# Performance work log

Hardware: AMD Instinct MI355X
Metric: run time of the kernel (lower is better)

## Reference

```python
import jax, jax.numpy as jnp
import numpy as np

N, B, T, C = 1024, 4, 12, 64
D, H, K, E = 64, 2, 3, 16384  # out_dim, gat heads, num_kernel, edges per kernel
NEG_SLOPE_ATTN = 0.2   # DGL GATConv default
NEG_SLOPE_ACT = 0.01   # nn.LeakyReLU default


def setup_inputs() -> dict:
    key = jax.random.key(0)
    ks = jax.random.split(key, 12)
    input_feature = jax.random.normal(ks[0], (B, N, T, C), dtype=jnp.float32)
    # edge lists per kernel, with self loops appended (dgl.add_self_loop)
    loops = jnp.broadcast_to(jnp.arange(N, dtype=jnp.int32), (K, N))
    src_idx = jnp.concatenate(
        [jax.random.randint(ks[1], (K, E), 0, N, dtype=jnp.int32), loops], axis=1)
    dst_idx = jnp.concatenate(
        [jax.random.randint(ks[2], (K, E), 0, N, dtype=jnp.int32), loops], axis=1)
    # GATConv params per kernel: fc (no bias), attn_l/attn_r, output bias
    fc_w = jax.random.normal(ks[3], (K, C, H * D), dtype=jnp.float32) * 0.1
    attn_l = jax.random.normal(ks[4], (K, H, D), dtype=jnp.float32) * 0.1
    attn_r = jax.random.normal(ks[5], (K, H, D), dtype=jnp.float32) * 0.1
    gat_bias = jax.random.normal(ks[6], (K, H * D), dtype=jnp.float32) * 0.02
    # per-kernel merge weight, init std 0.05 as in init_weight()
    weight = jax.random.normal(ks[7], (K,), dtype=jnp.float32) * 0.05
    # merge MLP: Linear(H*D -> D)
    merge_w = jax.random.normal(ks[8], (H * D, D), dtype=jnp.float32) * 0.05
    merge_b = jax.random.normal(ks[9], (D,), dtype=jnp.float32) * 0.02
    return {"input_feature": input_feature, "fc_w": fc_w, "attn_l": attn_l,
            "attn_r": attn_r, "gat_bias": gat_bias, "weight": weight,
            "merge_w": merge_w, "merge_b": merge_b,
            "src_idx": src_idx, "dst_idx": dst_idx}


def _gat_conv(x, fc_w, attn_l, attn_r, bias, src, dst):
    """DGL GATConv on feature x: [N,B,T,C] -> [N,B,T,H,D]."""
    feat = jnp.einsum('nbtc,ce->nbte', x, fc_w).reshape(N, B, T, H, D)
    el = jnp.einsum('nbthd,hd->nbth', feat, attn_l)  # [N,B,T,H]
    er = jnp.einsum('nbthd,hd->nbth', feat, attn_r)
    e = jax.nn.leaky_relu(el[src] + er[dst], NEG_SLOPE_ATTN)  # [Etot,B,T,H]
    # segment softmax over destination neighborhoods (self loops guarantee >=1 edge)
    emax = jax.ops.segment_max(e, dst, num_segments=N)
    a = jnp.exp(e - emax[dst])
    denom = jax.ops.segment_sum(a, dst, num_segments=N)
    alpha = a / denom[dst]
    msg = alpha[..., None] * feat[src]  # [Etot,B,T,H,D]
    rst = jax.ops.segment_sum(msg, dst, num_segments=N)
    return rst + bias.reshape(H, D)


def reference(input_feature, fc_w, attn_l, attn_r, gat_bias, weight,
              merge_w, merge_b, src_idx, dst_idx):
    x = jnp.transpose(input_feature, (1, 0, 2, 3))  # [N,B,T,C]
    result = jnp.zeros((N, B, T, H, D), dtype=x.dtype)
    for i in range(K):  # small fixed set of dilated kernels
        result = result + weight[i] * _gat_conv(
            x, fc_w[i], attn_l[i], attn_r[i], gat_bias[i], src_idx[i], dst_idx[i])
    merged = result.reshape(N, B, T, H * D) @ merge_w + merge_b  # [N,B,T,D]
    out = jax.nn.leaky_relu(merged, NEG_SLOPE_ACT) + x  # residual = Identity (C==D)
    return jnp.transpose(out, (1, 0, 2, 3))  # [B,N,T,D]
```

## Files before the change

kernel.cpp:

```cpp
#include <hip/hip_runtime.h>

#define NN   1024
#define TT   12
#define CC   64
#define DD   64
#define HH   2
#define KK   3
#define ETOT 17408
#define BT   48
#define BTH  96
#define HD   128
#define NODES (KK * NN + 1)
#define PADN  (KK * NN)
#define CSR_CAP (KK * ETOT + 12 * NN)
#define LOG2E 1.44269504f
#define MT   128
#define NBLK (NN * BT / MT)
#define EDGE_BLOCKS ((KK * ETOT + 255) / 256)
#define FEAT_BLOCKS (KK * NBLK)
#define NSL  12
#define RUNCAP 144

typedef __attribute__((ext_vector_type(8))) short s8v;
typedef __attribute__((ext_vector_type(4))) float f4v;

__device__ __forceinline__ float bf_lo(unsigned int u) {
    return __uint_as_float(u << 16);
}
__device__ __forceinline__ float bf_hi(unsigned int u) {
    return __uint_as_float(u & 0xFFFF0000u);
}
__device__ __forceinline__ unsigned short f2bf(float f) {
    unsigned int u = __float_as_uint(f);
    u += 0x7FFFu + ((u >> 16) & 1u);
    return (unsigned short)(u >> 16);
}
__device__ __forceinline__ unsigned int pack2(float a, float b) {
    return (unsigned int)f2bf(a) | ((unsigned int)f2bf(b) << 16);
}
__device__ __forceinline__ float rlf(float v, int lane) {
    return __int_as_float(__builtin_amdgcn_readlane(__float_as_int(v), lane));
}

__global__ __launch_bounds__(256) void aux_kernel(
    const int* __restrict__ dst_idx, int* __restrict__ counts,
    const float* __restrict__ fc_w, const float* __restrict__ attn_l,
    const float* __restrict__ attn_r, float* __restrict__ alc, float* __restrict__ arc,
    uint4* __restrict__ featp, float* __restrict__ elp)
{
    int bid = blockIdx.x;
    int t = threadIdx.x;
    if (bid < EDGE_BLOCKS) {
        int tid = bid * 256 + t;
        if (tid < KK * ETOT) {
            int k = tid / ETOT;
            atomicAdd(&counts[k * NN + dst_idx[tid]], 1);
        }
    } else {
        for (int item = t; item < KK * HH * CC; item += 256) {
            int kh = item >> 6, c = item & 63;
            int k = kh >> 1, h = kh & 1;
            float sl = 0.f, sr = 0.f;
            #pragma unroll
            for (int dd = 0; dd < 64; ++dd) {
                float wv = fc_w[k * CC * HD + c * HD + h * 64 + dd];
                sl = fmaf(wv, attn_l[k * HD + h * 64 + dd], sl);
                sr = fmaf(wv, attn_r[k * HD + h * 64 + dd], sr);
            }
            alc[item] = sl * LOG2E;
            arc[item] = sr * LOG2E;
        }
        for (int item = t; item < NSL * 64; item += 256)
            featp[((size_t)(item >> 6) * NODES + PADN) * 64 + (item & 63)] =
                make_uint4(0u, 0u, 0u, 0u);
        for (int item = t; item < NSL * 8; item += 256)
            elp[((size_t)(item >> 3) * NODES + PADN) * 8 + (item & 7)] = -1e30f;
    }
}

__global__ __launch_bounds__(1024) void scan_kernel(
    const int* __restrict__ counts,
    int4* __restrict__ segs, int* __restrict__ cursor, int* __restrict__ csr_comb)
{
    int n = threadIdx.x;
    int c0 = counts[n], c1 = counts[NN + n], c2 = counts[2 * NN + n];
    int p0 = (c0 + 3) & ~3, p1 = (c1 + 3) & ~3, p2 = (c2 + 3) & ~3;
    int tot = p0 + p1 + p2;
    __shared__ int buf[NN];
    buf[n] = tot;
    __syncthreads();
    for (int off = 1; off < NN; off <<= 1) {
        int v = (n >= off) ? buf[n - off] : 0;
        __syncthreads();
        buf[n] += v;
        __syncthreads();
    }
    int excl = buf[n] - tot;
    int4 sg;
    sg.x = excl; sg.y = excl + p0; sg.z = excl + p0 + p1; sg.w = excl + tot;
    segs[n] = sg;
    cursor[n] = sg.x;
    cursor[NN + n] = sg.y;
    cursor[2 * NN + n] = sg.z;
    for (int j = sg.x + c0; j < sg.y; ++j) csr_comb[j] = PADN;
    for (int j = sg.y + c1; j < sg.z; ++j) csr_comb[j] = PADN;
    for (int j = sg.z + c2; j < sg.w; ++j) csr_comb[j] = PADN;
}

__global__ __launch_bounds__(256) void feat_kernel(
    const float* __restrict__ x, const float* __restrict__ fc_w,
    uint4* __restrict__ featp)
{
    int kb = blockIdx.x;
    int k  = kb / NBLK;
    int m0 = (kb - k * NBLK) * MT;
    int t  = threadIdx.x;
    int w  = t >> 6, l = t & 63;

    __shared__ __align__(16) unsigned short As[128 * 64];
    __shared__ __align__(16) unsigned short Ws[128 * 64];

    #pragma unroll
    for (int rep = 0; rep < 4; ++rep) {
        int gid = t + 256 * rep;
        int row = gid >> 3, g = gid & 7;
        int m = m0 + row;
        int n = m / BT, bt = m - n * BT;
        int b = bt / TT, tt2 = bt - b * TT;
        const float* xr = &x[(((size_t)b * NN + n) * TT + tt2) * CC + g * 8];
        float4 v0 = *(const float4*)xr;
        float4 v1 = *(const float4*)(xr + 4);
        uint4 pk = { pack2(v0.x, v0.y), pack2(v0.z, v0.w),
                     pack2(v1.x, v1.y), pack2(v1.z, v1.w) };
        *(uint4*)((char*)As + row * 128 + ((g ^ (row & 7)) << 4)) = pk;
    }
    #pragma unroll
    for (int rep = 0; rep < 4; ++rep) {
        int gid = t + 256 * rep;
        int e = gid & 127, g = gid >> 7;
        float v[8];
        #pragma unroll
        for (int jj = 0; jj < 8; ++jj)
            v[jj] = fc_w[(size_t)k * CC * HD + (g * 8 + jj) * HD + e];
        uint4 pk = { pack2(v[0], v[1]), pack2(v[2], v[3]),
                     pack2(v[4], v[5]), pack2(v[6], v[7]) };
        *(uint4*)((char*)Ws + e * 128 + ((g ^ (e & 7)) << 4)) = pk;
    }
    __syncthreads();

    int Mw = (w & 1) * 64;
    int Nw = (w >> 1) * 64;
    int rsel = l & 15, ksel = l >> 4;

    f4v acc[4][4];
    #pragma unroll
    for (int mi = 0; mi < 4; ++mi)
        #pragma unroll
        for (int nf = 0; nf < 4; ++nf)
            acc[mi][nf] = (f4v){0.f, 0.f, 0.f, 0.f};

    s8v af[4][2], bf[4][2];
    #pragma unroll
    for (int mi = 0; mi < 4; ++mi)
        #pragma unroll
        for (int ks = 0; ks < 2; ++ks) {
            int row = Mw + mi * 16 + rsel;
            int g = ks * 4 + ksel;
            af[mi][ks] = *(const s8v*)((const char*)As + row * 128 + ((g ^ (row & 7)) << 4));
        }
    #pragma unroll
    for (int nf = 0; nf < 4; ++nf)
        #pragma unroll
        for (int ks = 0; ks < 2; ++ks) {
            int e = Nw + nf * 16 + rsel;
            int g = ks * 4 + ksel;
            bf[nf][ks] = *(const s8v*)((const char*)Ws + e * 128 + ((g ^ (e & 7)) << 4));
        }

    #pragma unroll
    for (int mi = 0; mi < 4; ++mi)
        #pragma unroll
        for (int nf = 0; nf < 4; ++nf) {
            acc[mi][nf] = __builtin_amdgcn_mfma_f32_16x16x32_bf16(
                af[mi][0], bf[nf][0], acc[mi][nf], 0, 0, 0);
            acc[mi][nf] = __builtin_amdgcn_mfma_f32_16x16x32_bf16(
                af[mi][1], bf[nf][1], acc[mi][nf], 0, 0, 0);
        }

    int i0 = (l >> 4) * 4;
    bool writer = ((l >> 4) & 1) == 0;
    #pragma unroll
    for (int mi = 0; mi < 4; ++mi) {
        int m = m0 + Mw + mi * 16 + i0;
        int n = m / BT, bt = m - n * BT;
        #pragma unroll
        for (int nf = 0; nf < 4; ++nf) {
            uint2 o = { pack2(acc[mi][nf][0], acc[mi][nf][1]),
                        pack2(acc[mi][nf][2], acc[mi][nf][3]) };
            unsigned int px = (unsigned int)__shfl_xor((int)o.x, 16, 64);
            unsigned int py = (unsigned int)__shfl_xor((int)o.y, 16, 64);
            if (writer) {
                int e = Nw + nf * 16 + (l & 15);
                int h = e >> 6, d = e & 63;
                int s = ((bt >> 3) << 1) + h;
                featp[((size_t)s * NODES + k * NN + n) * 64 + d] =
                    make_uint4(o.x, o.y, px, py);
            }
        }
    }
}

__global__ __launch_bounds__(256) void side_kernel(
    const int* __restrict__ src_idx, const int* __restrict__ dst_idx,
    int* __restrict__ cursor, int* __restrict__ csr_comb,
    const float* __restrict__ x,
    const float* __restrict__ alc, const float* __restrict__ arc,
    float* __restrict__ elp, float* __restrict__ er)
{
    int bid = blockIdx.x;
    int t = threadIdx.x;

    if (bid < EDGE_BLOCKS) {
        int tid = bid * 256 + t;
        if (tid < KK * ETOT) {
            int k = tid / ETOT;
            int pos = atomicAdd(&cursor[k * NN + dst_idx[tid]], 1);
            csr_comb[pos] = k * NN + src_idx[tid];
        }
        return;
    }

    __shared__ float x_lds[BT * CC];
    __shared__ float cl[KK * HH * CC];
    __shared__ float cr[KK * HH * CC];
    int n = bid - EDGE_BLOCKS;

    for (int i = t; i < BT * CC; i += 256) {
        int bt = i >> 6, c = i & 63;
        int b = bt / TT, tt = bt - b * TT;
        x_lds[i] = x[(((size_t)b * NN + n) * TT + tt) * CC + c];
    }
    for (int i = t; i < KK * HH * CC; i += 256) { cl[i] = alc[i]; cr[i] = arc[i]; }
    __syncthreads();

    if (t < BTH) {
        int hh = t / BT, bt = t - hh * BT;
        #pragma unroll
        for (int k = 0; k < KK; ++k) {
            const float* alp = &cl[(k * HH + hh) * CC];
            const float* arp = &cr[(k * HH + hh) * CC];
            float sl = 0.f, sr = 0.f;
            #pragma unroll
            for (int cc = 0; cc < CC; ++cc) {
                int c = (cc + bt) & 63;
                float xv = x_lds[bt * CC + c];
                sl = fmaf(xv, alp[c], sl);
                sr = fmaf(xv, arp[c], sr);
            }
            int s = ((bt >> 3) << 1) + hh;
            elp[((size_t)s * NODES + k * NN + n) * 8 + (bt & 7)] = sl;
            er[((size_t)(k * NN + n)) * BTH + t] = sr;
        }
    }
}

#define EFMA(F, LO, HI)                                        \
    r0 = fmaf((LO).x, bf_lo((F).x), r0);                       \
    r1 = fmaf((LO).y, bf_hi((F).x), r1);                       \
    r2 = fmaf((LO).z, bf_lo((F).y), r2);                       \
    r3 = fmaf((LO).w, bf_hi((F).y), r3);                       \
    r4 = fmaf((HI).x, bf_lo((F).z), r4);                       \
    r5 = fmaf((HI).y, bf_hi((F).z), r5);                       \
    r6 = fmaf((HI).z, bf_lo((F).w), r6);                       \
    r7 = fmaf((HI).w, bf_hi((F).w), r7);

#define PHASE1(JB, JE, KIDX, SCLO, SCHI) {                                     \
    int jb = (JB), je = (JE);                                                  \
    float erv = er[((size_t)((KIDX) * NN + n)) * BTH + h * BT + btg8 * 8 + btq];\
    float ss = 0.f;                                                            \
    for (int j0 = jb; j0 < je; j0 += 8) {                                      \
        int jj = j0 + joff;                                                    \
        float a = 0.f;                                                         \
        if (jj < je) {                                                         \
            int idx = csr_comb[jj];                                            \
            float ev = elp[(size_t)sbase8 + (size_t)idx * 8 + btq] + erv;      \
            ev = fmaxf(ev, ev * 0.2f);                                         \
            a = __builtin_amdgcn_exp2f(ev);                                    \
            alds[w][jj - base0][btq] = a;                                      \
        }                                                                      \
        ss += a;                                                               \
    }                                                                          \
    ss += __shfl_xor(ss, 8, 64);                                               \
    ss += __shfl_xor(ss, 16, 64);                                              \
    ss += __shfl_xor(ss, 32, 64);                                              \
    float wk_ = weight[KIDX];                                                  \
    SCLO = make_float4(wk_ * __builtin_amdgcn_rcpf(rlf(ss, 0)),                \
                       wk_ * __builtin_amdgcn_rcpf(rlf(ss, 1)),                \
                       wk_ * __builtin_amdgcn_rcpf(rlf(ss, 2)),                \
                       wk_ * __builtin_amdgcn_rcpf(rlf(ss, 3)));               \
    SCHI = make_float4(wk_ * __builtin_amdgcn_rcpf(rlf(ss, 4)),                \
                       wk_ * __builtin_amdgcn_rcpf(rlf(ss, 5)),                \
                       wk_ * __builtin_amdgcn_rcpf(rlf(ss, 6)),                \
                       wk_ * __builtin_amdgcn_rcpf(rlf(ss, 7))); }

#define PHASE2(JB, JE, SCLO, SCHI) {                                           \
    int jb = __builtin_amdgcn_readfirstlane(JB);                               \
    int je = __builtin_amdgcn_readfirstlane(JE);                               \
    float r0=0.f,r1=0.f,r2=0.f,r3=0.f,r4=0.f,r5=0.f,r6=0.f,r7=0.f;             \
    for (int jj = jb; jj < je; jj += 4) {                                      \
        int4 i4 = *(const int4*)&csr_comb[jj];                                 \
        int i0 = __builtin_amdgcn_readfirstlane(i4.x);                         \
        int i1 = __builtin_amdgcn_readfirstlane(i4.y);                         \
        int i2 = __builtin_amdgcn_readfirstlane(i4.z);                         \
        int i3 = __builtin_amdgcn_readfirstlane(i4.w);                         \
        uint4 f0 = fb[(size_t)i0 * 64];                                        \
        uint4 f1 = fb[(size_t)i1 * 64];                                        \
        uint4 f2 = fb[(size_t)i2 * 64];                                        \
        uint4 f3 = fb[(size_t)i3 * 64];                                        \
        float4 L0 = *(const float4*)&alds[w][jj - base0 + 0][0];               \
        float4 H0 = *(const float4*)&alds[w][jj - base0 + 0][4];               \
        float4 L1 = *(const float4*)&alds[w][jj - base0 + 1][0];               \
        float4 H1 = *(const float4*)&alds[w][jj - base0 + 1][4];               \
        float4 L2 = *(const float4*)&alds[w][jj - base0 + 2][0];               \
        float4 H2 = *(const float4*)&alds[w][jj - base0 + 2][4];               \
        float4 L3 = *(const float4*)&alds[w][jj - base0 + 3][0];               \
        float4 H3 = *(const float4*)&alds[w][jj - base0 + 3][4];               \
        EFMA(f0, L0, H0); EFMA(f1, L1, H1);                                    \
        EFMA(f2, L2, H2); EFMA(f3, L3, H3);                                    \
    }                                                                          \
    acc0 = fmaf(r0, (SCLO).x, acc0); acc1 = fmaf(r1, (SCLO).y, acc1);          \
    acc2 = fmaf(r2, (SCLO).z, acc2); acc3 = fmaf(r3, (SCLO).w, acc3);          \
    acc4 = fmaf(r4, (SCHI).x, acc4); acc5 = fmaf(r5, (SCHI).y, acc5);          \
    acc6 = fmaf(r6, (SCHI).z, acc6); acc7 = fmaf(r7, (SCHI).w, acc7); }

__global__ __launch_bounds__(256) void agg_kernel(
    const uint4* __restrict__ featp,
    const float* __restrict__ elp,
    const float* __restrict__ er,
    const int4* __restrict__ segs, const int* __restrict__ csr_comb,
    const float* __restrict__ gat_bias, const float* __restrict__ weight,
    unsigned short* __restrict__ gatb)
{
    int xcd = (int)blockIdx.x & 7;
    int q   = (int)blockIdx.x >> 3;
    int j   = q + 384 * xcd;
    int s   = j >> 8;
    int g   = j & 255;
    int w = threadIdx.x >> 6;
    int l = threadIdx.x & 63;
    int n = g * 4 + w;
    int btg8 = s >> 1, h = s & 1;
    int e = h * 64 + l;

    __shared__ __align__(16) float alds[4][RUNCAP][8];

    const uint4* fb = featp + (size_t)s * NODES * 64 + l;
    size_t sbase8 = (size_t)s * NODES * 8;
    int4 sg = segs[n];
    int base0 = __builtin_amdgcn_readfirstlane(sg.x);

    int joff = l >> 3, btq = l & 7;
    float acc0=0.f,acc1=0.f,acc2=0.f,acc3=0.f,acc4=0.f,acc5=0.f,acc6=0.f,acc7=0.f;
    float4 sclo, schi;

    PHASE1(sg.x, sg.y, 0, sclo, schi)
    PHASE2(sg.x, sg.y, sclo, schi)
    PHASE1(sg.y, sg.z, 1, sclo, schi)
    PHASE2(sg.y, sg.z, sclo, schi)
    PHASE1(sg.z, sg.w, 2, sclo, schi)
    PHASE2(sg.z, sg.w, sclo, schi)

    float wb = weight[0] * gat_bias[e] + weight[1] * gat_bias[HD + e]
             + weight[2] * gat_bias[2 * HD + e];
    acc0 += wb; acc1 += wb; acc2 += wb; acc3 += wb;
    acc4 += wb; acc5 += wb; acc6 += wb; acc7 += wb;

    size_t row = (size_t)n * BT + btg8 * 8;
    gatb[(row + 0) * HD + e] = f2bf(acc0);
    gatb[(row + 1) * HD + e] = f2bf(acc1);
    gatb[(row + 2) * HD + e] = f2bf(acc2);
    gatb[(row + 3) * HD + e] = f2bf(acc3);
    gatb[(row + 4) * HD + e] = f2bf(acc4);
    gatb[(row + 5) * HD + e] = f2bf(acc5);
    gatb[(row + 6) * HD + e] = f2bf(acc6);
    gatb[(row + 7) * HD + e] = f2bf(acc7);
}
#undef EFMA
#undef PHASE1
#undef PHASE2

__global__ __launch_bounds__(256) void merge_mfma_kernel(
    const unsigned short* __restrict__ gatb,
    const float* __restrict__ merge_w, const float* __restrict__ merge_b,
    const float* __restrict__ x, float* __restrict__ out)
{
    int m0 = blockIdx.x * 128;
    int t = threadIdx.x, w = t >> 6, l = t & 63;

    __shared__ __align__(16) unsigned short As[128 * 128];
    __shared__ __align__(16) unsigned short Bs[64 * 128];

    #pragma unroll
    for (int rep = 0; rep < 8; ++rep) {
        int gid = t + 256 * rep;
        int row = gid >> 4, gg = gid & 15;
        uint4 v = *(const uint4*)((const char*)gatb + ((size_t)(m0 + row)) * 256 + gg * 16);
        *(uint4*)((char*)As + row * 256 + ((gg ^ (row & 15)) << 4)) = v;
    }
    #pragma unroll
    for (int rep = 0; rep < 4; ++rep) {
        int gid = t + 256 * rep;
        int col = gid >> 4, gg = gid & 15;
        float v[8];
        #pragma unroll
        for (int jj = 0; jj < 8; ++jj)
            v[jj] = merge_w[(gg * 8 + jj) * DD + col];
        uint4 pk = { pack2(v[0], v[1]), pack2(v[2], v[3]),
                     pack2(v[4], v[5]), pack2(v[6], v[7]) };
        *(uint4*)((char*)Bs + col * 256 + ((gg ^ (col & 15)) << 4)) = pk;
    }
    __syncthreads();

    int Mw = (w & 1) * 64, Nw = (w >> 1) * 32;
    int rsel = l & 15, ksel = l >> 4;

    f4v acc[4][2];
    #pragma unroll
    for (int mi = 0; mi < 4; ++mi)
        #pragma unroll
        for (int nf = 0; nf < 2; ++nf)
            acc[mi][nf] = (f4v){0.f, 0.f, 0.f, 0.f};

    s8v af[4][4], bfr[2][4];
    #pragma unroll
    for (int mi = 0; mi < 4; ++mi)
        #pragma unroll
        for (int ks = 0; ks < 4; ++ks) {
            int row = Mw + mi * 16 + rsel;
            int g2 = ks * 4 + ksel;
            af[mi][ks] = *(const s8v*)((const char*)As + row * 256 + ((g2 ^ (row & 15)) << 4));
        }
    #pragma unroll
    for (int nf = 0; nf < 2; ++nf)
        #pragma unroll
        for (int ks = 0; ks < 4; ++ks) {
            int col = Nw + nf * 16 + rsel;
            int g2 = ks * 4 + ksel;
            bfr[nf][ks] = *(const s8v*)((const char*)Bs + col * 256 + ((g2 ^ (col & 15)) << 4));
        }

    #pragma unroll
    for (int mi = 0; mi < 4; ++mi)
        #pragma unroll
        for (int nf = 0; nf < 2; ++nf)
            #pragma unroll
            for (int ks = 0; ks < 4; ++ks)
                acc[mi][nf] = __builtin_amdgcn_mfma_f32_16x16x32_bf16(
                    af[mi][ks], bfr[nf][ks], acc[mi][nf], 0, 0, 0);

    int i0 = (l >> 4) * 4;
    #pragma unroll
    for (int mi = 0; mi < 4; ++mi) {
        int m = m0 + Mw + mi * 16 + i0;
        int n = m / BT, btb = m - n * BT;
        int b = btb / TT, t0 = btb - b * TT;
        #pragma unroll
        for (int nf = 0; nf < 2; ++nf) {
            int dd = Nw + nf * 16 + (l & 15);
            float mb = merge_b[dd];
            #pragma unroll
            for (int reg = 0; reg < 4; ++reg) {
                float mg = acc[mi][nf][reg] + mb;
                mg = mg > 0.f ? mg : mg * 0.01f;
                size_t oidx = (((size_t)b * NN + n) * TT + t0 + reg) * DD + dd;
                out[oidx] = mg + x[oidx];
            }
        }
    }
}

extern "C" void kernel_launch(void* const* d_in, const int* in_sizes, int n_in,
                              void* d_out, int out_size, void* d_ws, size_t ws_size,
                              hipStream_t stream)
{
    const float* x        = (const float*)d_in[0];
    const float* fc_w     = (const float*)d_in[1];
    const float* attn_l   = (const float*)d_in[2];
    const float* attn_r   = (const float*)d_in[3];
    const float* gat_bias = (const float*)d_in[4];
    const float* weight   = (const float*)d_in[5];
    const float* merge_w  = (const float*)d_in[6];
    const float* merge_b  = (const float*)d_in[7];
    const int*   src_idx  = (const int*)d_in[8];
    const int*   dst_idx  = (const int*)d_in[9];
    float*       out      = (float*)d_out;

    char* p = (char*)d_ws;
    auto carve = [&](size_t bytes) { char* r = p; p += (bytes + 15) & ~size_t(15); return r; };
    uint4* featp   = (uint4*)carve(sizeof(uint4) * (size_t)NSL * NODES * 64);
    unsigned short* gatb = (unsigned short*)carve(sizeof(unsigned short) * (size_t)NN * BT * HD);
    float* elp     = (float*)carve(sizeof(float) * (size_t)NSL * NODES * 8);
    float* er      = (float*)carve(sizeof(float) * (size_t)KK * NN * BTH);
    float* alc     = (float*)carve(sizeof(float) * KK * HH * CC);
    float* arc     = (float*)carve(sizeof(float) * KK * HH * CC);
    int*   counts  = (int*)carve(sizeof(int) * KK * NN);
    int*   cursor  = (int*)carve(sizeof(int) * KK * NN);
    int4*  segs    = (int4*)carve(sizeof(int4) * NN);
    int*   csr_comb= (int*)carve(sizeof(int) * (CSR_CAP + 80));

    hipMemsetAsync(counts, 0, sizeof(int) * KK * NN, stream);

    aux_kernel<<<EDGE_BLOCKS + 1, 256, 0, stream>>>(
        dst_idx, counts, fc_w, attn_l, attn_r, alc, arc, featp, elp);

    scan_kernel<<<1, 1024, 0, stream>>>(counts, segs, cursor, csr_comb);

    feat_kernel<<<FEAT_BLOCKS, 256, 0, stream>>>(x, fc_w, featp);

    side_kernel<<<EDGE_BLOCKS + NN, 256, 0, stream>>>(
        src_idx, dst_idx, cursor, csr_comb, x, alc, arc, elp, er);

    agg_kernel<<<NSL * 256, 256, 0, stream>>>(
        featp, elp, er, segs, csr_comb, gat_bias, weight, gatb);

    merge_mfma_kernel<<<NN * BT / 128, 256, 0, stream>>>(gatb, merge_w, merge_b, x, out);
}
```

Measured before the change: 117.9 us.

## Fuse attention-score and aggregation phases in agg kernel, dropping LDS staging

Merges the two per-segment passes (exp scores to LDS, then gather and FMA) into one loop. Scores stay in registers and are broadcast with readlane. CSR segments are now padded to multiples of 8 instead of 4 so the 8-edge inner loop needs no bounds check, and CSR capacity grows to match. This removes the LDS buffer, its round trips and the second csr read, at the cost of more readlane ops and more padded edges.

```diff
diff --git a/kernel.cpp b/kernel.cpp
--- a/kernel.cpp
+++ b/kernel.cpp
@@ -12,14 +12,13 @@
 #define HD   128
 #define NODES (KK * NN + 1)
 #define PADN  (KK * NN)
-#define CSR_CAP (KK * ETOT + 12 * NN)
+#define CSR_CAP (KK * ETOT + 21 * NN)
 #define LOG2E 1.44269504f
 #define MT   128
 #define NBLK (NN * BT / MT)
 #define EDGE_BLOCKS ((KK * ETOT + 255) / 256)
 #define FEAT_BLOCKS (KK * NBLK)
 #define NSL  12
-#define RUNCAP 144
 
 typedef __attribute__((ext_vector_type(8))) short s8v;
 typedef __attribute__((ext_vector_type(4))) float f4v;
@@ -84,7 +83,7 @@
 {
     int n = threadIdx.x;
     int c0 = counts[n], c1 = counts[NN + n], c2 = counts[2 * NN + n];
-    int p0 = (c0 + 3) & ~3, p1 = (c1 + 3) & ~3, p2 = (c2 + 3) & ~3;
+    int p0 = (c0 + 7) & ~7, p1 = (c1 + 7) & ~7, p2 = (c2 + 7) & ~7;
     int tot = p0 + p1 + p2;
     __shared__ int buf[NN];
     buf[n] = tot;
@@ -264,74 +263,44 @@
     }
 }
 
-#define EFMA(F, LO, HI)                                        \
-    r0 = fmaf((LO).x, bf_lo((F).x), r0);                       \
-    r1 = fmaf((LO).y, bf_hi((F).x), r1);                       \
-    r2 = fmaf((LO).z, bf_lo((F).y), r2);                       \
-    r3 = fmaf((LO).w, bf_hi((F).y), r3);                       \
-    r4 = fmaf((HI).x, bf_lo((F).z), r4);                       \
-    r5 = fmaf((HI).y, bf_hi((F).z), r5);                       \
-    r6 = fmaf((HI).z, bf_lo((F).w), r6);                       \
-    r7 = fmaf((HI).w, bf_hi((F).w), r7);
-
-#define PHASE1(JB, JE, KIDX, SCLO, SCHI) {                                     \
-    int jb = (JB), je = (JE);                                                  \
+#define SEG(JB, JE, KIDX) {                                                    \
+    int jb = __builtin_amdgcn_readfirstlane(JB);                               \
+    int je = __builtin_amdgcn_readfirstlane(JE);                               \
     float erv = er[((size_t)((KIDX) * NN + n)) * BTH + h * BT + btg8 * 8 + btq];\
     float ss = 0.f;                                                            \
+    float r0=0.f,r1=0.f,r2=0.f,r3=0.f,r4=0.f,r5=0.f,r6=0.f,r7=0.f;             \
     for (int j0 = jb; j0 < je; j0 += 8) {                                      \
-        int jj = j0 + joff;                                                    \
-        float a = 0.f;                                                         \
-        if (jj < je) {                                                         \
-            int idx = csr_comb[jj];                                            \
-            float ev = elp[(size_t)sbase8 + (size_t)idx * 8 + btq] + erv;      \
-            ev = fmaxf(ev, ev * 0.2f);                                         \
-            a = __builtin_amdgcn_exp2f(ev);                                    \
-            alds[w][jj - base0][btq] = a;                                      \
+        int idx = csr_comb[j0 + joff];                                         \
+        float ev = elp[sbase8 + (size_t)idx * 8 + btq] + erv;                  \
+        ev = fmaxf(ev, ev * 0.2f);                                             \
+        float a = __builtin_amdgcn_exp2f(ev);                                  \
+        ss += a;                                                               \
+        _Pragma("unroll")                                                      \
+        for (int u = 0; u < 8; ++u) {                                          \
+            int iu = __builtin_amdgcn_readlane(idx, u * 8);                    \
+            uint4 f = fb[(size_t)iu * 64];                                     \
+            r0 = fmaf(rlf(a, u * 8 + 0), bf_lo(f.x), r0);                      \
+            r1 = fmaf(rlf(a, u * 8 + 1), bf_hi(f.x), r1);                      \
+            r2 = fmaf(rlf(a, u * 8 + 2), bf_lo(f.y), r2);                      \
+            r3 = fmaf(rlf(a, u * 8 + 3), bf_hi(f.y), r3);                      \
+            r4 = fmaf(rlf(a, u * 8 + 4), bf_lo(f.z), r4);                      \
+            r5 = fmaf(rlf(a, u * 8 + 5), bf_hi(f.z), r5);                      \
+            r6 = fmaf(rlf(a, u * 8 + 6), bf_lo(f.w), r6);                      \
+            r7 = fmaf(rlf(a, u * 8 + 7), bf_hi(f.w), r7);                      \
         }                                                                      \
-        ss += a;                                                               \
     }                                                                          \
     ss += __shfl_xor(ss, 8, 64);                                               \
     ss += __shfl_xor(ss, 16, 64);                                              \
     ss += __shfl_xor(ss, 32, 64);                                              \
     float wk_ = weight[KIDX];                                                  \
-    SCLO = make_float4(wk_ * __builtin_amdgcn_rcpf(rlf(ss, 0)),                \
-                       wk_ * __builtin_amdgcn_rcpf(rlf(ss, 1)),                \
-                       wk_ * __builtin_amdgcn_rcpf(rlf(ss, 2)),                \
-                       wk_ * __builtin_amdgcn_rcpf(rlf(ss, 3)));               \
-    SCHI = make_float4(wk_ * __builtin_amdgcn_rcpf(rlf(ss, 4)),                \
-                       wk_ * __builtin_amdgcn_rcpf(rlf(ss, 5)),                \
-                       wk_ * __builtin_amdgcn_rcpf(rlf(ss, 6)),                \
-                       wk_ * __builtin_amdgcn_rcpf(rlf(ss, 7))); }
-
-#define PHASE2(JB, JE, SCLO, SCHI) {                                           \
-    int jb = __builtin_amdgcn_readfirstlane(JB);                               \
-    int je = __builtin_amdgcn_readfirstlane(JE);                               \
-    float r0=0.f,r1=0.f,r2=0.f,r3=0.f,r4=0.f,r5=0.f,r6=0.f,r7=0.f;             \
-    for (int jj = jb; jj < je; jj += 4) {                                      \
-        int4 i4 = *(const int4*)&csr_comb[jj];                                 \
-        int i0 = __builtin_amdgcn_readfirstlane(i4.x);                         \
-        int i1 = __builtin_amdgcn_readfirstlane(i4.y);                         \
-        int i2 = __builtin_amdgcn_readfirstlane(i4.z);                         \
-        int i3 = __builtin_amdgcn_readfirstlane(i4.w);                         \
-        uint4 f0 = fb[(size_t)i0 * 64];                                        \
-        uint4 f1 = fb[(size_t)i1 * 64];                                        \
-        uint4 f2 = fb[(size_t)i2 * 64];                                        \
-        uint4 f3 = fb[(size_t)i3 * 64];                                        \
-        float4 L0 = *(const float4*)&alds[w][jj - base0 + 0][0];               \
-        float4 H0 = *(const float4*)&alds[w][jj - base0 + 0][4];               \
-        float4 L1 = *(const float4*)&alds[w][jj - base0 + 1][0];               \
-        float4 H1 = *(const float4*)&alds[w][jj - base0 + 1][4];               \
-        float4 L2 = *(const float4*)&alds[w][jj - base0 + 2][0];               \
-        float4 H2 = *(const float4*)&alds[w][jj - base0 + 2][4];               \
-        float4 L3 = *(const float4*)&alds[w][jj - base0 + 3][0];               \
-        float4 H3 = *(const float4*)&alds[w][jj - base0 + 3][4];               \
-        EFMA(f0, L0, H0); EFMA(f1, L1, H1);                                    \
-        EFMA(f2, L2, H2); EFMA(f3, L3, H3);                                    \
-    }                                                                          \
-    acc0 = fmaf(r0, (SCLO).x, acc0); acc1 = fmaf(r1, (SCLO).y, acc1);          \
-    acc2 = fmaf(r2, (SCLO).z, acc2); acc3 = fmaf(r3, (SCLO).w, acc3);          \
-    acc4 = fmaf(r4, (SCHI).x, acc4); acc5 = fmaf(r5, (SCHI).y, acc5);          \
-    acc6 = fmaf(r6, (SCHI).z, acc6); acc7 = fmaf(r7, (SCHI).w, acc7); }
+    acc0 = fmaf(r0, wk_ * __builtin_amdgcn_rcpf(rlf(ss, 0)), acc0);            \
+    acc1 = fmaf(r1, wk_ * __builtin_amdgcn_rcpf(rlf(ss, 1)), acc1);            \
+    acc2 = fmaf(r2, wk_ * __builtin_amdgcn_rcpf(rlf(ss, 2)), acc2);            \
+    acc3 = fmaf(r3, wk_ * __builtin_amdgcn_rcpf(rlf(ss, 3)), acc3);            \
+    acc4 = fmaf(r4, wk_ * __builtin_amdgcn_rcpf(rlf(ss, 4)), acc4);            \
+    acc5 = fmaf(r5, wk_ * __builtin_amdgcn_rcpf(rlf(ss, 5)), acc5);            \
+    acc6 = fmaf(r6, wk_ * __builtin_amdgcn_rcpf(rlf(ss, 6)), acc6);            \
+    acc7 = fmaf(r7, wk_ * __builtin_amdgcn_rcpf(rlf(ss, 7)), acc7); }
 
 __global__ __launch_bounds__(256) void agg_kernel(
     const uint4* __restrict__ featp,
@@ -352,23 +321,16 @@
     int btg8 = s >> 1, h = s & 1;
     int e = h * 64 + l;
 
-    __shared__ __align__(16) float alds[4][RUNCAP][8];
-
     const uint4* fb = featp + (size_t)s * NODES * 64 + l;
     size_t sbase8 = (size_t)s * NODES * 8;
     int4 sg = segs[n];
-    int base0 = __builtin_amdgcn_readfirstlane(sg.x);
 
     int joff = l >> 3, btq = l & 7;
     float acc0=0.f,acc1=0.f,acc2=0.f,acc3=0.f,acc4=0.f,acc5=0.f,acc6=0.f,acc7=0.f;
-    float4 sclo, schi;
-
-    PHASE1(sg.x, sg.y, 0, sclo, schi)
-    PHASE2(sg.x, sg.y, sclo, schi)
-    PHASE1(sg.y, sg.z, 1, sclo, schi)
-    PHASE2(sg.y, sg.z, sclo, schi)
-    PHASE1(sg.z, sg.w, 2, sclo, schi)
-    PHASE2(sg.z, sg.w, sclo, schi)
+
+    SEG(sg.x, sg.y, 0)
+    SEG(sg.y, sg.z, 1)
+    SEG(sg.z, sg.w, 2)
 
     float wb = weight[0] * gat_bias[e] + weight[1] * gat_bias[HD + e]
              + weight[2] * gat_bias[2 * HD + e];
@@ -385,9 +347,7 @@
     gatb[(row + 6) * HD + e] = f2bf(acc6);
     gatb[(row + 7) * HD + e] = f2bf(acc7);
 }
-#undef EFMA
-#undef PHASE1
-#undef PHASE2
+#undef SEG
 
 __global__ __launch_bounds__(256) void merge_mfma_kernel(
     const unsigned short* __restrict__ gatb,
```

Measured after the change: 121.7 us (median of 2 runs). 3.3% more time.
